# Optimization experiments

Measured on AMD Instinct MI355X. Metric: run time of the kernel, lower is better.

Reference implementation:

```python
import jax, jax.numpy as jnp
import numpy as np
jax.config.update("jax_enable_x64", True)

N, VDIM, D = 65536, 3, 256
EPS = 1e-3


def setup_inputs() -> dict:
    key = jax.random.key(0)
    k1, _ = jax.random.split(key)
    inp = jax.random.normal(k1, (N, VDIM, D), dtype=jnp.float32)
    weight = jnp.ones((D,), dtype=jnp.float32)
    return {"input": inp, "weight": weight}


def _symsqrtinv(covar, eps):
    # covar: (N, 3, 3) symmetric PSD (fp64). Matches torch .svd() semantics.
    u, s, vt = jnp.linalg.svd(covar)
    v = jnp.swapaxes(vt, -1, -2)  # torch.svd returns V, jnp returns V^T
    thresh = s.max(-1, keepdims=True) * s.shape[-1] * jnp.finfo(s.dtype).eps
    good = s > thresh
    inv = jnp.where(good, 1.0 / jnp.sqrt(s + eps), 0.0)  # drop bad components
    return (v * inv[..., None, :]) @ vt  # V diag(inv) V^T


def reference(input, weight):
    x = input.astype(jnp.float64)
    x = x - x.mean(-1, keepdims=True)                      # mean-center over width d
    reg = jnp.diag(jnp.asarray([1.0, 2.0, 3.0], dtype=x.dtype))
    covar = (x @ jnp.swapaxes(x, -1, -2)) / D + EPS * reg  # (N, 3, 3)
    covar_sqrtinv = _symsqrtinv(covar, EPS)
    out = (covar_sqrtinv @ x).astype(weight.dtype) * weight.reshape(1, 1, D)
    return out
```

## Files before the change

kernel.cpp:

```cpp
#include <hip/hip_runtime.h>


namespace {

constexpr int kD = 256;
constexpr float kEps = 1e-3f;
constexpr int kNSIters = 8;

typedef float f4 __attribute__((ext_vector_type(4)));

__device__ __forceinline__ void symmul(const float* M, const float* N, float* P) {
    P[0] = M[0]*N[0] + M[1]*N[1] + M[2]*N[2];
    P[1] = M[0]*N[1] + M[1]*N[3] + M[2]*N[4];
    P[2] = M[0]*N[2] + M[1]*N[4] + M[2]*N[5];
    P[3] = M[1]*N[1] + M[3]*N[3] + M[4]*N[4];
    P[4] = M[1]*N[2] + M[3]*N[4] + M[4]*N[5];
    P[5] = M[2]*N[2] + M[4]*N[4] + M[5]*N[5];
}

__global__ __launch_bounds__(256) void eqln_kernel(const float* __restrict__ in,
                                                   const float* __restrict__ wptr,
                                                   float* __restrict__ out,
                                                   int nrows) {
    const int tid     = threadIdx.x;
    const int lane_in = tid & 31;
    const int row     = blockIdx.x * (blockDim.x >> 5) + (tid >> 5);
    if (row >= nrows) return;

    const size_t base = (size_t)row * (3 * kD);
    const int coff = lane_in * 4;

    f4 x[3][2];
    #pragma unroll
    for (int v = 0; v < 3; ++v)
        #pragma unroll
        for (int j = 0; j < 2; ++j)
            x[v][j] = __builtin_nontemporal_load(
                (const f4*)(in + base + v * kD + j * 128 + coff));

    float s[9] = {0.f, 0.f, 0.f, 0.f, 0.f, 0.f, 0.f, 0.f, 0.f};
    #pragma unroll
    for (int j = 0; j < 2; ++j) {
        const f4 a = x[0][j];
        const f4 b = x[1][j];
        const f4 c = x[2][j];
        #pragma unroll
        for (int k = 0; k < 4; ++k) {
            s[0] += a[k];      s[1] += b[k];      s[2] += c[k];
            s[3] += a[k]*a[k]; s[4] += a[k]*b[k]; s[5] += a[k]*c[k];
            s[6] += b[k]*b[k]; s[7] += b[k]*c[k]; s[8] += c[k]*c[k];
        }
    }

    #pragma unroll
    for (int off = 16; off > 0; off >>= 1) {
        #pragma unroll
        for (int i = 0; i < 9; ++i) s[i] += __shfl_xor(s[i], off, 64);
    }

    const float inv_d = 1.0f / (float)kD;
    const float m0 = s[0] * inv_d, m1 = s[1] * inv_d, m2 = s[2] * inv_d;

    float B[6];
    B[0] = s[3] * inv_d - m0 * m0 + 2.0f * kEps;
    B[1] = s[4] * inv_d - m0 * m1;
    B[2] = s[5] * inv_d - m0 * m2;
    B[3] = s[6] * inv_d - m1 * m1 + 3.0f * kEps;
    B[4] = s[7] * inv_d - m1 * m2;
    B[5] = s[8] * inv_d - m2 * m2 + 4.0f * kEps;

    const float tr  = B[0] + B[3] + B[5];
    const float itr = 1.0f / tr;
    float Y[6] = {B[0]*itr, B[1]*itr, B[2]*itr, B[3]*itr, B[4]*itr, B[5]*itr};
    float Z[6] = {1.0f, 0.0f, 0.0f, 1.0f, 0.0f, 1.0f};

    #pragma unroll
    for (int it = 0; it < kNSIters; ++it) {
        float W[6], T[6], Yn[6], Zn[6];
        symmul(Z, Y, W);
        T[0] = 1.5f - 0.5f * W[0];
        T[1] = -0.5f * W[1];
        T[2] = -0.5f * W[2];
        T[3] = 1.5f - 0.5f * W[3];
        T[4] = -0.5f * W[4];
        T[5] = 1.5f - 0.5f * W[5];
        symmul(Y, T, Yn);
        symmul(T, Z, Zn);
        #pragma unroll
        for (int i = 0; i < 6; ++i) { Y[i] = Yn[i]; Z[i] = Zn[i]; }
    }

    const float sc  = 1.0f / sqrtf(tr);
    const float M00 = Z[0] * sc, M01 = Z[1] * sc, M02 = Z[2] * sc;
    const float M11 = Z[3] * sc, M12 = Z[4] * sc, M22 = Z[5] * sc;

    #pragma unroll
    for (int j = 0; j < 2; ++j) {
        const f4 wv = *(const f4*)(wptr + j * 128 + coff);
        const f4 a  = x[0][j];
        const f4 b  = x[1][j];
        const f4 c  = x[2][j];
        f4 r0, r1, r2;
        #pragma unroll
        for (int k = 0; k < 4; ++k) {
            const float a0 = a[k] - m0;
            const float a1 = b[k] - m1;
            const float a2 = c[k] - m2;
            r0[k] = (M00 * a0 + M01 * a1 + M02 * a2) * wv[k];
            r1[k] = (M01 * a0 + M11 * a1 + M12 * a2) * wv[k];
            r2[k] = (M02 * a0 + M12 * a1 + M22 * a2) * wv[k];
        }
        __builtin_nontemporal_store(r0, (f4*)(out + base + 0 * kD + j * 128 + coff));
        __builtin_nontemporal_store(r1, (f4*)(out + base + 1 * kD + j * 128 + coff));
        __builtin_nontemporal_store(r2, (f4*)(out + base + 2 * kD + j * 128 + coff));
    }
}

}

extern "C" void kernel_launch(void* const* d_in, const int* in_sizes, int n_in,
                              void* d_out, int out_size, void* d_ws, size_t ws_size,
                              hipStream_t stream) {
    (void)n_in; (void)d_ws; (void)ws_size; (void)out_size;
    const float* in   = (const float*)d_in[0];
    const float* wght = (const float*)d_in[1];
    float* out = (float*)d_out;

    const int nrows = in_sizes[0] / (3 * kD);
    const int rows_per_block = 256 / 32;
    const int blocks = (nrows + rows_per_block - 1) / rows_per_block;

    eqln_kernel<<<blocks, 256, 0, stream>>>(in, wght, out, nrows);
}
```

Measured before the change: 319.0 us.

## Offload per-row Newton-Schulz solve to one thread per row via shared memory

Previously each 32-lane group redundantly ran the 8-iteration Newton-Schulz inverse square root on every lane. Now lane 0 of each group writes the means and covariance to shared memory, the first 8 threads of the block each solve one row's 3x3 matrix, and every group reads the result back after a second barrier. The aim is to remove redundant ALU work and register pressure, and launch bounds now request 8 blocks per CU. In exchange it adds two block-wide barriers and serializes the solve, which can stall the memory-bound streaming.

```diff
diff --git a/kernel.cpp b/kernel.cpp
--- a/kernel.cpp
+++ b/kernel.cpp
@@ -6,6 +6,7 @@
 constexpr int kD = 256;
 constexpr float kEps = 1e-3f;
 constexpr int kNSIters = 8;
+constexpr int kRowsPerBlock = 8;
 
 typedef float f4 __attribute__((ext_vector_type(4)));
 
@@ -18,101 +19,123 @@
     P[5] = M[2]*N[2] + M[4]*N[4] + M[5]*N[5];
 }
 
-__global__ __launch_bounds__(256) void eqln_kernel(const float* __restrict__ in,
-                                                   const float* __restrict__ wptr,
-                                                   float* __restrict__ out,
-                                                   int nrows) {
+__global__ __launch_bounds__(256, 8) void eqln_kernel(const float* __restrict__ in,
+                                                      const float* __restrict__ wptr,
+                                                      float* __restrict__ out,
+                                                      int nrows) {
     const int tid     = threadIdx.x;
     const int lane_in = tid & 31;
-    const int row     = blockIdx.x * (blockDim.x >> 5) + (tid >> 5);
-    if (row >= nrows) return;
+    const int grp     = tid >> 5;
+    const int row     = blockIdx.x * kRowsPerBlock + grp;
 
+    __shared__ float sm[kRowsPerBlock][12];
+
+    const bool valid = row < nrows;
     const size_t base = (size_t)row * (3 * kD);
     const int coff = lane_in * 4;
 
     f4 x[3][2];
-    #pragma unroll
-    for (int v = 0; v < 3; ++v)
+    float s[9] = {0.f, 0.f, 0.f, 0.f, 0.f, 0.f, 0.f, 0.f, 0.f};
+    if (valid) {
         #pragma unroll
-        for (int j = 0; j < 2; ++j)
-            x[v][j] = __builtin_nontemporal_load(
-                (const f4*)(in + base + v * kD + j * 128 + coff));
+        for (int v = 0; v < 3; ++v)
+            #pragma unroll
+            for (int j = 0; j < 2; ++j)
+                x[v][j] = __builtin_nontemporal_load(
+                    (const f4*)(in + base + v * kD + j * 128 + coff));
 
-    float s[9] = {0.f, 0.f, 0.f, 0.f, 0.f, 0.f, 0.f, 0.f, 0.f};
-    #pragma unroll
-    for (int j = 0; j < 2; ++j) {
-        const f4 a = x[0][j];
-        const f4 b = x[1][j];
-        const f4 c = x[2][j];
         #pragma unroll
-        for (int k = 0; k < 4; ++k) {
-            s[0] += a[k];      s[1] += b[k];      s[2] += c[k];
-            s[3] += a[k]*a[k]; s[4] += a[k]*b[k]; s[5] += a[k]*c[k];
-            s[6] += b[k]*b[k]; s[7] += b[k]*c[k]; s[8] += c[k]*c[k];
+        for (int j = 0; j < 2; ++j) {
+            const f4 a = x[0][j];
+            const f4 b = x[1][j];
+            const f4 c = x[2][j];
+            #pragma unroll
+            for (int k = 0; k < 4; ++k) {
+                s[0] += a[k];      s[1] += b[k];      s[2] += c[k];
+                s[3] += a[k]*a[k]; s[4] += a[k]*b[k]; s[5] += a[k]*c[k];
+                s[6] += b[k]*b[k]; s[7] += b[k]*c[k]; s[8] += c[k]*c[k];
+            }
+        }
+
+        #pragma unroll
+        for (int off = 16; off > 0; off >>= 1) {
+            #pragma unroll
+            for (int i = 0; i < 9; ++i) s[i] += __shfl_xor(s[i], off, 64);
+        }
+
+        if (lane_in == 0) {
+            const float inv_d = 1.0f / (float)kD;
+            const float m0 = s[0] * inv_d, m1 = s[1] * inv_d, m2 = s[2] * inv_d;
+            sm[grp][0] = m0;
+            sm[grp][1] = m1;
+            sm[grp][2] = m2;
+            sm[grp][3] = s[3] * inv_d - m0 * m0 + 2.0f * kEps;
+            sm[grp][4] = s[4] * inv_d - m0 * m1;
+            sm[grp][5] = s[5] * inv_d - m0 * m2;
+            sm[grp][6] = s[6] * inv_d - m1 * m1 + 3.0f * kEps;
+            sm[grp][7] = s[7] * inv_d - m1 * m2;
+            sm[grp][8] = s[8] * inv_d - m2 * m2 + 4.0f * kEps;
         }
     }
+    __syncthreads();
 
-    #pragma unroll
-    for (int off = 16; off > 0; off >>= 1) {
+    if (tid < kRowsPerBlock && (blockIdx.x * kRowsPerBlock + tid) < nrows) {
+        float B[6];
         #pragma unroll
-        for (int i = 0; i < 9; ++i) s[i] += __shfl_xor(s[i], off, 64);
+        for (int i = 0; i < 6; ++i) B[i] = sm[tid][3 + i];
+
+        const float tr  = B[0] + B[3] + B[5];
+        const float itr = 1.0f / tr;
+        float Y[6] = {B[0]*itr, B[1]*itr, B[2]*itr, B[3]*itr, B[4]*itr, B[5]*itr};
+        float Z[6] = {1.0f, 0.0f, 0.0f, 1.0f, 0.0f, 1.0f};
+
+        #pragma unroll
+        for (int it = 0; it < kNSIters; ++it) {
+            float W[6], T[6], Yn[6], Zn[6];
+            symmul(Z, Y, W);
+            T[0] = 1.5f - 0.5f * W[0];
+            T[1] = -0.5f * W[1];
+            T[2] = -0.5f * W[2];
+            T[3] = 1.5f - 0.5f * W[3];
+            T[4] = -0.5f * W[4];
+            T[5] = 1.5f - 0.5f * W[5];
+            symmul(Y, T, Yn);
+            symmul(T, Z, Zn);
+            #pragma unroll
+            for (int i = 0; i < 6; ++i) { Y[i] = Yn[i]; Z[i] = Zn[i]; }
+        }
+
+        const float sc = 1.0f / sqrtf(tr);
+        #pragma unroll
+        for (int i = 0; i < 6; ++i) sm[tid][3 + i] = Z[i] * sc;
     }
+    __syncthreads();
 
-    const float inv_d = 1.0f / (float)kD;
-    const float m0 = s[0] * inv_d, m1 = s[1] * inv_d, m2 = s[2] * inv_d;
+    if (valid) {
+        const float m0  = sm[grp][0], m1 = sm[grp][1], m2 = sm[grp][2];
+        const float M00 = sm[grp][3], M01 = sm[grp][4], M02 = sm[grp][5];
+        const float M11 = sm[grp][6], M12 = sm[grp][7], M22 = sm[grp][8];
 
-    float B[6];
-    B[0] = s[3] * inv_d - m0 * m0 + 2.0f * kEps;
-    B[1] = s[4] * inv_d - m0 * m1;
-    B[2] = s[5] * inv_d - m0 * m2;
-    B[3] = s[6] * inv_d - m1 * m1 + 3.0f * kEps;
-    B[4] = s[7] * inv_d - m1 * m2;
-    B[5] = s[8] * inv_d - m2 * m2 + 4.0f * kEps;
-
-    const float tr  = B[0] + B[3] + B[5];
-    const float itr = 1.0f / tr;
-    float Y[6] = {B[0]*itr, B[1]*itr, B[2]*itr, B[3]*itr, B[4]*itr, B[5]*itr};
-    float Z[6] = {1.0f, 0.0f, 0.0f, 1.0f, 0.0f, 1.0f};
-
-    #pragma unroll
-    for (int it = 0; it < kNSIters; ++it) {
-        float W[6], T[6], Yn[6], Zn[6];
-        symmul(Z, Y, W);
-        T[0] = 1.5f - 0.5f * W[0];
-        T[1] = -0.5f * W[1];
-        T[2] = -0.5f * W[2];
-        T[3] = 1.5f - 0.5f * W[3];
-        T[4] = -0.5f * W[4];
-        T[5] = 1.5f - 0.5f * W[5];
-        symmul(Y, T, Yn);
-        symmul(T, Z, Zn);
         #pragma unroll
-        for (int i = 0; i < 6; ++i) { Y[i] = Yn[i]; Z[i] = Zn[i]; }
-    }
-
-    const float sc  = 1.0f / sqrtf(tr);
-    const float M00 = Z[0] * sc, M01 = Z[1] * sc, M02 = Z[2] * sc;
-    const float M11 = Z[3] * sc, M12 = Z[4] * sc, M22 = Z[5] * sc;
-
-    #pragma unroll
-    for (int j = 0; j < 2; ++j) {
-        const f4 wv = *(const f4*)(wptr + j * 128 + coff);
-        const f4 a  = x[0][j];
-        const f4 b  = x[1][j];
-        const f4 c  = x[2][j];
-        f4 r0, r1, r2;
-        #pragma unroll
-        for (int k = 0; k < 4; ++k) {
-            const float a0 = a[k] - m0;
-            const float a1 = b[k] - m1;
-            const float a2 = c[k] - m2;
-            r0[k] = (M00 * a0 + M01 * a1 + M02 * a2) * wv[k];
-            r1[k] = (M01 * a0 + M11 * a1 + M12 * a2) * wv[k];
-            r2[k] = (M02 * a0 + M12 * a1 + M22 * a2) * wv[k];
+        for (int j = 0; j < 2; ++j) {
+            const f4 wv = *(const f4*)(wptr + j * 128 + coff);
+            const f4 a  = x[0][j];
+            const f4 b  = x[1][j];
+            const f4 c  = x[2][j];
+            f4 r0, r1, r2;
+            #pragma unroll
+            for (int k = 0; k < 4; ++k) {
+                const float a0 = a[k] - m0;
+                const float a1 = b[k] - m1;
+                const float a2 = c[k] - m2;
+                r0[k] = (M00 * a0 + M01 * a1 + M02 * a2) * wv[k];
+                r1[k] = (M01 * a0 + M11 * a1 + M12 * a2) * wv[k];
+                r2[k] = (M02 * a0 + M12 * a1 + M22 * a2) * wv[k];
+            }
+            __builtin_nontemporal_store(r0, (f4*)(out + base + 0 * kD + j * 128 + coff));
+            __builtin_nontemporal_store(r1, (f4*)(out + base + 1 * kD + j * 128 + coff));
+            __builtin_nontemporal_store(r2, (f4*)(out + base + 2 * kD + j * 128 + coff));
         }
-        __builtin_nontemporal_store(r0, (f4*)(out + base + 0 * kD + j * 128 + coff));
-        __builtin_nontemporal_store(r1, (f4*)(out + base + 1 * kD + j * 128 + coff));
-        __builtin_nontemporal_store(r2, (f4*)(out + base + 2 * kD + j * 128 + coff));
     }
 }
 
@@ -127,8 +150,7 @@
     float* out = (float*)d_out;
 
     const int nrows = in_sizes[0] / (3 * kD);
-    const int rows_per_block = 256 / 32;
-    const int blocks = (nrows + rows_per_block - 1) / rows_per_block;
+    const int blocks = (nrows + kRowsPerBlock - 1) / kRowsPerBlock;
 
     eqln_kernel<<<blocks, 256, 0, stream>>>(in, wght, out, nrows);
 }
```

Result: slower. 347.7 us (+9.0%).
